# Optimization experiments

Measured on AMD Instinct MI355X. Metric: run time of the kernel, lower is better.

The kernel has to match this reference:

```python
import jax, jax.numpy as jnp
import numpy as np

MIN_EXP = 1    # log2(min_window=2)
MAX_EXP = 10   # log2(max_window=1024)
OUT_LEN = 16384  # reconstructed signal length L; encoded len = L*(1 - 2**-MAX_EXP)


def setup_inputs() -> dict:
    key = jax.random.key(0)
    k1, k2, k3 = jax.random.split(key, 3)
    B = 2048
    enc_len = OUT_LEN * (2 ** (1 - MIN_EXP)) - OUT_LEN // (2 ** MAX_EXP)  # 16368
    weights_len = 2 * (2 ** MAX_EXP) - 1  # 2047
    stdev = 1.0 / np.sqrt(weights_len)
    data = jax.random.normal(k1, (B, enc_len), dtype=jnp.float32)
    weights = jax.random.uniform(k2, (weights_len,), dtype=jnp.float32, minval=-stdev, maxval=stdev)
    bias = jax.random.uniform(k3, (MAX_EXP,), dtype=jnp.float32, minval=-stdev, maxval=stdev)
    return {"data": data, "weights": weights, "bias": bias}


def reference(data, weights, bias):
    """Transposed time-scale convolution: for each dyadic scale e (window w=2**e),
    the shared kernel weights[w-1:2w-1] is overlap-added (stride == window, so the
    windows tile the output exactly) scaled by that scale's coefficients, summed
    across scales, with a per-scale bias."""
    B = data.shape[0]
    out = jnp.zeros((B, OUT_LEN), dtype=data.dtype)
    offset = 0
    for e in range(MIN_EXP, MAX_EXP + 1):
        w = 2 ** e
        n = OUT_LEN // w                      # number of windows at this scale
        kern = weights[w - 1: 2 * w - 1]      # [w] kernel for this scale
        coeffs = data[:, offset: offset + n]  # [B, n]
        offset += n
        # transposed conv with stride = kernel size: outer product then tile
        contrib = (coeffs[:, :, None] * kern[None, None, :]).reshape(B, OUT_LEN)
        out = out + contrib + bias[e - 1]
    return out
```

## Files before the change

### kernel.cpp

```cpp
#include <hip/hip_runtime.h>

#define TSC_OUT_LEN 16384
#define TSC_ENC_LEN 16368
#define TSC_ROWS 16

__device__ __forceinline__ float tsc_rfl(float x) {
    return __uint_as_float(__builtin_amdgcn_readfirstlane(__float_as_uint(x)));
}

struct TscLd {
    float4 d1;
    float2 d2;
    float  c3;
    float  c4, c5, c6, c7, c8;
    float  c9, c10;
};

__global__ __launch_bounds__(256, 4) void tsc_transpose_kernel(
    const float* __restrict__ data,
    const float* __restrict__ weights,
    const float* __restrict__ bias,
    float* __restrict__ out)
{
    __shared__ float wl[2048];
    const int tid = threadIdx.x;
    for (int i = tid; i < 2047; i += 256) wl[i + 1] = weights[i];
    __syncthreads();

    const int tile = blockIdx.x & 7;
    const int rg   = blockIdx.x >> 3;
    const int j0   = (tile << 11) + (tid << 3);

    float bs = 0.0f;
#pragma unroll
    for (int i = 0; i < 10; ++i) bs += bias[i];

    const float w1a = tsc_rfl(wl[2]), w1b = tsc_rfl(wl[3]);
    const float w2a = tsc_rfl(wl[4]), w2b = tsc_rfl(wl[5]);
    const float w2c = tsc_rfl(wl[6]), w2d = tsc_rfl(wl[7]);
    float w3[8];
#pragma unroll
    for (int i = 0; i < 8; ++i) w3[i] = tsc_rfl(wl[8 + i]);

    float4 wa[7], wb[7];
#pragma unroll
    for (int e = 4; e <= 10; ++e) {
        const int w  = 1 << e;
        const int kb = w + (j0 & (w - 1));
        wa[e - 4] = *reinterpret_cast<const float4*>(&wl[kb]);
        wb[e - 4] = *reinterpret_cast<const float4*>(&wl[kb + 4]);
    }

    const int i1 = (j0 >> 1);
    const int i2 = 8192  + (j0 >> 2);
    const int i3 = 12288 + (j0 >> 3);
    const int i4 = 14336 + (j0 >> 4);
    const int i5 = 15360 + (j0 >> 5);
    const int i6 = 15872 + (j0 >> 6);
    const int i7 = 16128 + (j0 >> 7);
    const int i8 = 16256 + (j0 >> 8);
    const int i9  = 16320 + __builtin_amdgcn_readfirstlane(j0 >> 9);
    const int i10 = 16352 + __builtin_amdgcn_readfirstlane(j0 >> 10);

    const float* drow = data + (size_t)rg * TSC_ROWS * TSC_ENC_LEN;
    float*       orow = out  + (size_t)rg * TSC_ROWS * TSC_OUT_LEN + j0;

    auto issue = [&](const float* dp, TscLd& L) {
        L.d1  = *reinterpret_cast<const float4*>(dp + i1);
        L.d2  = *reinterpret_cast<const float2*>(dp + i2);
        L.c3  = dp[i3];
        L.c4  = dp[i4];
        L.c5  = dp[i5];
        L.c6  = dp[i6];
        L.c7  = dp[i7];
        L.c8  = dp[i8];
        L.c9  = dp[i9];
        L.c10 = dp[i10];
    };

    auto compute_store = [&](const TscLd& L, float* op) {
        float a0 = bs, a1 = bs, a2 = bs, a3 = bs;
        float a4 = bs, a5 = bs, a6 = bs, a7 = bs;
        a0 = fmaf(L.d1.x, w1a, a0); a1 = fmaf(L.d1.x, w1b, a1);
        a2 = fmaf(L.d1.y, w1a, a2); a3 = fmaf(L.d1.y, w1b, a3);
        a4 = fmaf(L.d1.z, w1a, a4); a5 = fmaf(L.d1.z, w1b, a5);
        a6 = fmaf(L.d1.w, w1a, a6); a7 = fmaf(L.d1.w, w1b, a7);
        a0 = fmaf(L.d2.x, w2a, a0); a1 = fmaf(L.d2.x, w2b, a1);
        a2 = fmaf(L.d2.x, w2c, a2); a3 = fmaf(L.d2.x, w2d, a3);
        a4 = fmaf(L.d2.y, w2a, a4); a5 = fmaf(L.d2.y, w2b, a5);
        a6 = fmaf(L.d2.y, w2c, a6); a7 = fmaf(L.d2.y, w2d, a7);
        a0 = fmaf(L.c3, w3[0], a0); a1 = fmaf(L.c3, w3[1], a1);
        a2 = fmaf(L.c3, w3[2], a2); a3 = fmaf(L.c3, w3[3], a3);
        a4 = fmaf(L.c3, w3[4], a4); a5 = fmaf(L.c3, w3[5], a5);
        a6 = fmaf(L.c3, w3[6], a6); a7 = fmaf(L.c3, w3[7], a7);
#define TSC_E(c, i) \
        a0 = fmaf(c, wa[i].x, a0); a1 = fmaf(c, wa[i].y, a1); \
        a2 = fmaf(c, wa[i].z, a2); a3 = fmaf(c, wa[i].w, a3); \
        a4 = fmaf(c, wb[i].x, a4); a5 = fmaf(c, wb[i].y, a5); \
        a6 = fmaf(c, wb[i].z, a6); a7 = fmaf(c, wb[i].w, a7);
        TSC_E(L.c4, 0)
        TSC_E(L.c5, 1)
        TSC_E(L.c6, 2)
        TSC_E(L.c7, 3)
        TSC_E(L.c8, 4)
        TSC_E(L.c9, 5)
        TSC_E(L.c10, 6)
#undef TSC_E
        float4* o4 = reinterpret_cast<float4*>(op);
        o4[0] = make_float4(a0, a1, a2, a3);
        o4[1] = make_float4(a4, a5, a6, a7);
    };

    TscLd L0, L1;
    issue(drow, L0);
#pragma unroll 1
    for (int r = 0; r < TSC_ROWS; r += 2) {
        issue(drow + TSC_ENC_LEN, L1);
        compute_store(L0, orow);
        if (r + 2 < TSC_ROWS) issue(drow + 2 * TSC_ENC_LEN, L0);
        compute_store(L1, orow + TSC_OUT_LEN);
        drow += 2 * TSC_ENC_LEN;
        orow += 2 * TSC_OUT_LEN;
    }
}

extern "C" void kernel_launch(void* const* d_in, const int* in_sizes, int n_in,
                              void* d_out, int out_size, void* d_ws, size_t ws_size,
                              hipStream_t stream) {
    const float* data    = (const float*)d_in[0];
    const float* weights = (const float*)d_in[1];
    const float* bias    = (const float*)d_in[2];
    float* out = (float*)d_out;

    const int B = in_sizes[0] / TSC_ENC_LEN;
    dim3 grid((B / TSC_ROWS) * 8);
    dim3 block(256);
    tsc_transpose_kernel<<<grid, block, 0, stream>>>(data, weights, bias, out);
}
```

Baseline: 245.9 us.

## Stage coarse-scale coefficients through double-buffered LDS instead of per-lane global loads

Coarse-scale coefficients (scales 3..10) were loaded by each lane with scalar global reads that are heavily redundant across lanes. Now half of the block cooperatively loads the tile's coarse coefficients as contiguous float4/float2 chunks, writes them into a double-buffered shared-memory tail array, and each thread reads its values from LDS. This is meant to cut the number of vector memory instructions and redundant cache traffic. In exchange it adds workgroup barriers every row and LDS reads, which could stall the load/store pipelining.

```diff
diff --git a/kernel.cpp b/kernel.cpp
--- a/kernel.cpp
+++ b/kernel.cpp
@@ -3,6 +3,12 @@
 #define TSC_OUT_LEN 16384
 #define TSC_ENC_LEN 16368
 #define TSC_ROWS 16
+
+#define TSC_BARRIER() do { \
+    asm volatile("s_waitcnt lgkmcnt(0)" ::: "memory"); \
+    __builtin_amdgcn_s_barrier(); \
+    asm volatile("" ::: "memory"); \
+} while (0)
 
 __device__ __forceinline__ float tsc_rfl(float x) {
     return __uint_as_float(__builtin_amdgcn_readfirstlane(__float_as_uint(x)));
@@ -11,9 +17,6 @@
 struct TscLd {
     float4 d1;
     float2 d2;
-    float  c3;
-    float  c4, c5, c6, c7, c8;
-    float  c9, c10;
 };
 
 __global__ __launch_bounds__(256, 4) void tsc_transpose_kernel(
@@ -23,6 +26,7 @@
     float* __restrict__ out)
 {
     __shared__ float wl[2048];
+    __shared__ __align__(16) float tail[2][512];
     const int tid = threadIdx.x;
     for (int i = tid; i < 2047; i += 256) wl[i + 1] = weights[i];
     __syncthreads();
@@ -52,33 +56,66 @@
     }
 
     const int i1 = (j0 >> 1);
-    const int i2 = 8192  + (j0 >> 2);
-    const int i3 = 12288 + (j0 >> 3);
-    const int i4 = 14336 + (j0 >> 4);
-    const int i5 = 15360 + (j0 >> 5);
-    const int i6 = 15872 + (j0 >> 6);
-    const int i7 = 16128 + (j0 >> 7);
-    const int i8 = 16256 + (j0 >> 8);
-    const int i9  = 16320 + __builtin_amdgcn_readfirstlane(j0 >> 9);
-    const int i10 = 16352 + __builtin_amdgcn_readfirstlane(j0 >> 10);
+    const int i2 = 8192 + (j0 >> 2);
+
+    const int t3  = tid;
+    const int t4  = 256 + (tid >> 1);
+    const int t5  = 384 + (tid >> 2);
+    const int t6  = 448 + (tid >> 3);
+    const int t7  = 480 + (tid >> 4);
+    const int t8  = 496 + (tid >> 5);
+    const int t9  = 504 + (tid >> 6);
+    const int t10 = 508 + (tid >> 7);
+
+    int sg = 0;
+    if (tid < 128) {
+        int e, bslot;
+        if      (tid < 64)  { e = 3;  bslot = 0;   }
+        else if (tid < 96)  { e = 4;  bslot = 64;  }
+        else if (tid < 112) { e = 5;  bslot = 96;  }
+        else if (tid < 120) { e = 6;  bslot = 112; }
+        else if (tid < 124) { e = 7;  bslot = 120; }
+        else if (tid < 126) { e = 8;  bslot = 124; }
+        else if (tid < 127) { e = 9;  bslot = 126; }
+        else                { e = 10; bslot = 127; }
+        const int off_e = TSC_OUT_LEN - (TSC_OUT_LEN >> (e - 1));
+        sg = off_e + tile * (2048 >> e) + ((tid - bslot) << 2);
+    }
 
     const float* drow = data + (size_t)rg * TSC_ROWS * TSC_ENC_LEN;
     float*       orow = out  + (size_t)rg * TSC_ROWS * TSC_OUT_LEN + j0;
 
-    auto issue = [&](const float* dp, TscLd& L) {
-        L.d1  = *reinterpret_cast<const float4*>(dp + i1);
-        L.d2  = *reinterpret_cast<const float2*>(dp + i2);
-        L.c3  = dp[i3];
-        L.c4  = dp[i4];
-        L.c5  = dp[i5];
-        L.c6  = dp[i6];
-        L.c7  = dp[i7];
-        L.c8  = dp[i8];
-        L.c9  = dp[i9];
-        L.c10 = dp[i10];
+    auto issue_d = [&](const float* dp, TscLd& L) {
+        L.d1 = *reinterpret_cast<const float4*>(dp + i1);
+        L.d2 = *reinterpret_cast<const float2*>(dp + i2);
+    };
+    auto load_stage = [&](const float* dp) -> float4 {
+        float4 v = make_float4(0.f, 0.f, 0.f, 0.f);
+        if (tid < 127) {
+            v = *reinterpret_cast<const float4*>(dp + sg);
+        } else if (tid == 127) {
+            const float2 h = *reinterpret_cast<const float2*>(dp + sg);
+            v.x = h.x; v.y = h.y;
+        }
+        return v;
+    };
+    auto write_stage = [&](const float4& v, float* tb) {
+        if (tid < 127) {
+            *reinterpret_cast<float4*>(tb + (tid << 2)) = v;
+        } else if (tid == 127) {
+            tb[508] = v.x; tb[509] = v.y;
+        }
     };
 
-    auto compute_store = [&](const TscLd& L, float* op) {
+    auto compute_store = [&](const TscLd& L, const float* tb, float* op) {
+        const float c3  = tb[t3];
+        const float c4  = tb[t4];
+        const float c5  = tb[t5];
+        const float c6  = tb[t6];
+        const float c7  = tb[t7];
+        const float c8  = tb[t8];
+        const float c9  = tb[t9];
+        const float c10 = tb[t10];
         float a0 = bs, a1 = bs, a2 = bs, a3 = bs;
         float a4 = bs, a5 = bs, a6 = bs, a7 = bs;
         a0 = fmaf(L.d1.x, w1a, a0); a1 = fmaf(L.d1.x, w1b, a1);
@@ -89,22 +126,22 @@
         a2 = fmaf(L.d2.x, w2c, a2); a3 = fmaf(L.d2.x, w2d, a3);
         a4 = fmaf(L.d2.y, w2a, a4); a5 = fmaf(L.d2.y, w2b, a5);
         a6 = fmaf(L.d2.y, w2c, a6); a7 = fmaf(L.d2.y, w2d, a7);
-        a0 = fmaf(L.c3, w3[0], a0); a1 = fmaf(L.c3, w3[1], a1);
-        a2 = fmaf(L.c3, w3[2], a2); a3 = fmaf(L.c3, w3[3], a3);
-        a4 = fmaf(L.c3, w3[4], a4); a5 = fmaf(L.c3, w3[5], a5);
-        a6 = fmaf(L.c3, w3[6], a6); a7 = fmaf(L.c3, w3[7], a7);
+        a0 = fmaf(c3, w3[0], a0); a1 = fmaf(c3, w3[1], a1);
+        a2 = fmaf(c3, w3[2], a2); a3 = fmaf(c3, w3[3], a3);
+        a4 = fmaf(c3, w3[4], a4); a5 = fmaf(c3, w3[5], a5);
+        a6 = fmaf(c3, w3[6], a6); a7 = fmaf(c3, w3[7], a7);
 #define TSC_E(c, i) \
         a0 = fmaf(c, wa[i].x, a0); a1 = fmaf(c, wa[i].y, a1); \
         a2 = fmaf(c, wa[i].z, a2); a3 = fmaf(c, wa[i].w, a3); \
         a4 = fmaf(c, wb[i].x, a4); a5 = fmaf(c, wb[i].y, a5); \
         a6 = fmaf(c, wb[i].z, a6); a7 = fmaf(c, wb[i].w, a7);
-        TSC_E(L.c4, 0)
-        TSC_E(L.c5, 1)
-        TSC_E(L.c6, 2)
-        TSC_E(L.c7, 3)
-        TSC_E(L.c8, 4)
-        TSC_E(L.c9, 5)
-        TSC_E(L.c10, 6)
+        TSC_E(c4, 0)
+        TSC_E(c5, 1)
+        TSC_E(c6, 2)
+        TSC_E(c7, 3)
+        TSC_E(c8, 4)
+        TSC_E(c9, 5)
+        TSC_E(c10, 6)
 #undef TSC_E
         float4* o4 = reinterpret_cast<float4*>(op);
         o4[0] = make_float4(a0, a1, a2, a3);
@@ -112,13 +149,30 @@
     };
 
     TscLd L0, L1;
-    issue(drow, L0);
+    float4 S0, S1;
+    issue_d(drow,               L0);  S0 = load_stage(drow);
+    issue_d(drow + TSC_ENC_LEN, L1);  S1 = load_stage(drow + TSC_ENC_LEN);
+    write_stage(S0, tail[0]);
+    TSC_BARRIER();
+
 #pragma unroll 1
     for (int r = 0; r < TSC_ROWS; r += 2) {
-        issue(drow + TSC_ENC_LEN, L1);
-        compute_store(L0, orow);
-        if (r + 2 < TSC_ROWS) issue(drow + 2 * TSC_ENC_LEN, L0);
-        compute_store(L1, orow + TSC_OUT_LEN);
+        write_stage(S1, tail[1]);
+        compute_store(L0, tail[0], orow);
+        if (r + 2 < TSC_ROWS) {
+            issue_d(drow + 2 * TSC_ENC_LEN, L0);
+            S0 = load_stage(drow + 2 * TSC_ENC_LEN);
+        }
+        TSC_BARRIER();
+
+        if (r + 2 < TSC_ROWS) write_stage(S0, tail[0]);
+        compute_store(L1, tail[1], orow + TSC_OUT_LEN);
+        if (r + 3 < TSC_ROWS) {
+            issue_d(drow + 3 * TSC_ENC_LEN, L1);
+            S1 = load_stage(drow + 3 * TSC_ENC_LEN);
+        }
+        TSC_BARRIER();
+
         drow += 2 * TSC_ENC_LEN;
         orow += 2 * TSC_OUT_LEN;
     }
```

Measured after the change: 243.9 us. Within noise of the previous version (-0.8%).
